# Kernel optimization log

Hardware: AMD Instinct MI355X
Metric: run time of the kernel (lower is better)

## Reference

```python
import jax, jax.numpy as jnp
import numpy as np

B, N, F_ = 4, 2048, 512
H = 8
D = F_ // H


def setup_inputs() -> dict:
    key = jax.random.key(0)
    ks = jax.random.split(key, 9)
    s = 1.0 / np.sqrt(F_)
    return {
        "x": jax.random.normal(ks[0], (B, N, F_), dtype=jnp.float32),
        "Wq": jax.random.normal(ks[1], (F_, F_), dtype=jnp.float32) * s,
        "bq": jax.random.normal(ks[2], (F_,), dtype=jnp.float32) * 0.01,
        "Wk": jax.random.normal(ks[3], (F_, F_), dtype=jnp.float32) * s,
        "bk": jax.random.normal(ks[4], (F_,), dtype=jnp.float32) * 0.01,
        "Wv": jax.random.normal(ks[5], (F_, F_), dtype=jnp.float32) * s,
        "bv": jax.random.normal(ks[6], (F_,), dtype=jnp.float32) * 0.01,
        "Wo": jax.random.normal(ks[7], (F_, F_), dtype=jnp.float32) * s,
        "bo": jax.random.normal(ks[8], (F_,), dtype=jnp.float32) * 0.01,
    }


def reference(x, Wq, bq, Wk, bk, Wv, bv, Wo, bo):
    b, n, f = x.shape
    h, d = H, f // H
    # projections -> [b, h, n, d]
    q = (x @ Wq + bq).reshape(b, n, h, d).transpose(0, 2, 1, 3)
    k = (x @ Wk + bk).reshape(b, n, h, d).transpose(0, 2, 1, 3)
    v = (x @ Wv + bv).reshape(b, n, h, d).transpose(0, 2, 1, 3)
    # NOTE: module scales by sqrt(feats), not sqrt(head_dim)
    sqrt_d = jnp.asarray(f, x.dtype) ** 0.5
    score = jax.nn.softmax(jnp.einsum('bhif,bhjf->bhij', q, k) / sqrt_d, axis=-1)
    attn = jnp.einsum('bhij,bhjf->bihf', score, v).reshape(b, n, f)
    return attn @ Wo + bo
```

## Files before the change

kernel.cpp:

```cpp
#include <hip/hip_runtime.h>


typedef _Float16 f16;
typedef _Float16 f16x2 __attribute__((ext_vector_type(2)));
typedef _Float16 f16x4 __attribute__((ext_vector_type(4)));
typedef _Float16 f16x8 __attribute__((ext_vector_type(8)));
typedef float f32x4 __attribute__((ext_vector_type(4)));

#define MFMA16(a, b, c) __builtin_amdgcn_mfma_f32_16x16x32_f16((a), (b), (c), 0, 0, 0)
#if __has_builtin(__builtin_amdgcn_exp2f)
#define EXP2(x) __builtin_amdgcn_exp2f(x)
#else
#define EXP2(x) exp2f(x)
#endif
#define GLLDS16(gp, lp)                                                    \
  __builtin_amdgcn_global_load_lds(                                        \
      (const __attribute__((address_space(1))) unsigned int*)(gp),         \
      (__attribute__((address_space(3))) unsigned int*)(lp), 16, 0, 0)

#define QSCALE 0.0637587f

__global__ __launch_bounds__(256) void k_cvt_x(const float* __restrict__ x,
                                               f16* __restrict__ xb, int n4) {
  int i = blockIdx.x * 256 + threadIdx.x;
  const int stride = gridDim.x * 256;
  const float4* xp = (const float4*)x;
  f16x4* op = (f16x4*)xb;
  for (; i < n4; i += stride) {
    float4 v = xp[i];
    f16x4 o = {(f16)v.x, (f16)v.y, (f16)v.z, (f16)v.w};
    op[i] = o;
  }
}

__global__ __launch_bounds__(256) void k_cvt_w(const float* __restrict__ Wq,
                                               const float* __restrict__ Wk,
                                               const float* __restrict__ Wv,
                                               const float* __restrict__ Wo,
                                               f16* __restrict__ wt) {
  const int w = blockIdx.y;
  const float* W = (w == 0) ? Wq : (w == 1) ? Wk : (w == 2) ? Wv : Wo;
  const int j0 = (blockIdx.x >> 4) * 32;
  const int k0 = (blockIdx.x & 15) * 32;
  __shared__ float tl[32][33];
  const int tx = threadIdx.x & 31, ty = threadIdx.x >> 5;
#pragma unroll
  for (int i = 0; i < 32; i += 8)
    tl[ty + i][tx] = W[(size_t)(k0 + ty + i) * 512 + j0 + tx];
  __syncthreads();
#pragma unroll
  for (int i = 0; i < 32; i += 8)
    wt[(size_t)w * 262144 + (size_t)(j0 + ty + i) * 512 + (k0 + tx)] =
        (f16)tl[tx][ty + i];
}

template <int BN, int MODE>
__global__ __launch_bounds__(256) void k_gemm(
    const f16* __restrict__ A, const f16* __restrict__ Wb3,
    const float* __restrict__ bias0, const float* __restrict__ bias1,
    const float* __restrict__ bias2, f16* __restrict__ oQ, f16* __restrict__ oK,
    f16* __restrict__ oV, float* __restrict__ oOut) {
  __shared__ __align__(16) f16 a_lds[128 * 64];
  __shared__ __align__(16) f16 b_lds[BN * 64];
  const int t = threadIdx.x;
  const int lane = t & 63, wid = t >> 6;
  const int l15 = lane & 15, l4 = lane >> 4;
  constexpr int MT = (BN == 128) ? 4 : 2;
  const int mbase = (BN == 128) ? (wid >> 1) * 64 : wid * 32;
  const int nbase = (BN == 128) ? (wid & 1) * 64 : 0;
  const int m0 = blockIdx.x * 128;
  const int by = blockIdx.y;
  const int wsel = (MODE == 0) ? (by >> 2) : 0;
  const int n0l = (MODE == 0) ? ((by & 3) * 128) : (by * (BN == 64 ? 64 : 128));
  const f16* Wt = Wb3 + (size_t)wsel * 262144;

  const int srow = t >> 3;
  const int sswz = ((t & 7) ^ (srow & 7)) * 8;
  const f16* Ag = A + (size_t)(m0 + srow) * 512 + sswz;
  const f16* Bg = Wt + (size_t)(n0l + srow) * 512 + sswz;

  f32x4 acc[MT][4];
  const f32x4 z4 = {0.f, 0.f, 0.f, 0.f};
#pragma unroll
  for (int i = 0; i < MT; i++)
#pragma unroll
    for (int j = 0; j < 4; j++) acc[i][j] = z4;

  for (int k0 = 0; k0 < 512; k0 += 64) {
#pragma unroll
    for (int i = 0; i < 4; i++)
      GLLDS16(Ag + (size_t)i * 16384 + k0, &a_lds[i * 2048 + wid * 512]);
#pragma unroll
    for (int i = 0; i < BN / 32; i++)
      GLLDS16(Bg + (size_t)i * 16384 + k0, &b_lds[i * 2048 + wid * 512]);
    __syncthreads();
#pragma unroll
    for (int ks = 0; ks < 2; ks++) {
      const int rs = ((ks * 4 + l4) ^ (l15 & 7)) * 8;
      f16x8 af[MT], bf[4];
#pragma unroll
      for (int mt = 0; mt < MT; mt++)
        af[mt] = *(const f16x8*)&a_lds[(mbase + mt * 16 + l15) * 64 + rs];
#pragma unroll
      for (int nt = 0; nt < 4; nt++)
        bf[nt] = *(const f16x8*)&b_lds[(nbase + nt * 16 + l15) * 64 + rs];
      __builtin_amdgcn_s_setprio(1);
#pragma unroll
      for (int mt = 0; mt < MT; mt++)
#pragma unroll
        for (int nt = 0; nt < 4; nt++)
          acc[mt][nt] = MFMA16(af[mt], bf[nt], acc[mt][nt]);
      __builtin_amdgcn_s_setprio(0);
    }
    __syncthreads();
  }

  if (MODE == 1) {
#pragma unroll
    for (int mt = 0; mt < MT; mt++)
#pragma unroll
      for (int nt = 0; nt < 4; nt++) {
        const int row = m0 + mbase + mt * 16 + l4 * 4;
        const int col = n0l + nbase + nt * 16 + l15;
        const float bv = bias0[col];
#pragma unroll
        for (int r = 0; r < 4; r++)
          oOut[(size_t)(row + r) * 512 + col] = acc[mt][nt][r] + bv;
      }
  } else {
#pragma unroll
    for (int mt = 0; mt < MT; mt++)
#pragma unroll
      for (int nt = 0; nt < 4; nt++) {
        const int colg = by * 128 + nbase + nt * 16 + l15;
        const int w = colg >> 9, jj = colg & 511;
        const int h = jj >> 6, d = jj & 63;
        const float* bp = (w == 0) ? bias0 : (w == 1) ? bias1 : bias2;
        const float bv = bp[jj];
        const float scl = (w == 0) ? QSCALE : 1.0f;
        const int rowg = m0 + mbase + mt * 16 + l4 * 4;
        const int b = rowg >> 11, nn = rowg & 2047;
        if (w == 2) {
          const size_t vb = ((size_t)(b * 8 + h) * 64 + d) * 2048 + nn;
#pragma unroll
          for (int r = 0; r < 4; r++)
            oV[vb + r] = (f16)(acc[mt][nt][r] + bv);
        } else {
          f16* op = (w == 0) ? oQ : oK;
          const size_t base = ((size_t)(b * 8 + h) * 2048 + nn) * 64 + d;
#pragma unroll
          for (int r = 0; r < 4; r++)
            op[base + (size_t)r * 64] = (f16)((acc[mt][nt][r] + bv) * scl);
        }
      }
  }
}

__global__ __launch_bounds__(128, 4) void k_attn(const f16* __restrict__ Q,
                                                 const f16* __restrict__ K,
                                                 const f16* __restrict__ Vt,
                                                 f16* __restrict__ CTX) {
  __shared__ __align__(16) f16 k_lds[2][4096];
  __shared__ __align__(16) f16 v_lds[2][4096];
  const int t = threadIdx.x, wid = t >> 6, lane = t & 63;
  const int l15 = lane & 15, l4 = lane >> 4;
  const int bid = blockIdx.x;
  const int bh = (bid & 7) * 4 + (bid >> 8);
  const int qb = (bid >> 3) & 31;
  const int q0 = qb * 64 + wid * 32;
  const size_t kvb = (size_t)bh * (2048 * 64);

  f16x8 qf[2][2];
#pragma unroll
  for (int g = 0; g < 2; g++)
#pragma unroll
    for (int ks = 0; ks < 2; ks++)
      qf[g][ks] = *(const f16x8*)&Q[kvb + (size_t)(q0 + g * 16 + l15) * 64 +
                                    ks * 32 + l4 * 8];

  f32x4 oa[2][4];
  f32x4 lacc[2];
  const f32x4 z4 = {0.f, 0.f, 0.f, 0.f};
#pragma unroll
  for (int g = 0; g < 2; g++) {
    lacc[g] = z4;
#pragma unroll
    for (int dt = 0; dt < 4; dt++) oa[g][dt] = z4;
  }
  const f16 one = (f16)1.0f;
  const f16x8 ones = {one, one, one, one, one, one, one, one};

  const int kswz = ((lane & 7) ^ (lane >> 3)) * 8;
  const f16* Kgp[4];
  const f16* Vgp[4];
#pragma unroll
  for (int i = 0; i < 4; i++) {
    const int L = i * 16 + wid * 8 + (lane >> 3);
    const int pr = (L & 0x20) | ((L & 0x0C) << 1) | ((L & 0x10) >> 2) | (L & 3);
    Kgp[i] = K + kvb + (size_t)pr * 64 + kswz;
    Vgp[i] = Vt + kvb + (size_t)L * 2048 + kswz;
  }

#pragma unroll
  for (int i = 0; i < 4; i++) {
    GLLDS16(Kgp[i], &k_lds[0][i * 1024 + wid * 512]);
    GLLDS16(Vgp[i], &v_lds[0][i * 1024 + wid * 512]);
  }
  __syncthreads();

  int cur = 0;
  for (int it = 0; it < 32; ++it) {
    if (it < 31) {
      const size_t kb = (size_t)(it + 1) * 4096;
      const size_t vb = (size_t)(it + 1) * 64;
#pragma unroll
      for (int i = 0; i < 4; i++) {
        GLLDS16(Kgp[i] + kb, &k_lds[cur ^ 1][i * 1024 + wid * 512]);
        GLLDS16(Vgp[i] + vb, &v_lds[cur ^ 1][i * 1024 + wid * 512]);
      }
    }

    f32x4 st[2][4];
#pragma unroll
    for (int g = 0; g < 2; g++)
#pragma unroll
      for (int w = 0; w < 4; w++) st[g][w] = z4;
    const f16* kl = k_lds[cur];
#pragma unroll
    for (int ks = 0; ks < 2; ks++) {
      const int rs = ((ks * 4 + l4) ^ (l15 & 7)) * 8;
      f16x8 kf[4];
#pragma unroll
      for (int w = 0; w < 4; w++)
        kf[w] = *(const f16x8*)&kl[(w * 16 + l15) * 64 + rs];
      __builtin_amdgcn_s_setprio(1);
#pragma unroll
      for (int w = 0; w < 4; w++) {
        st[0][w] = MFMA16(kf[w], qf[0][ks], st[0][w]);
        st[1][w] = MFMA16(kf[w], qf[1][ks], st[1][w]);
      }
      __builtin_amdgcn_s_setprio(0);
    }

    f16x8 pa[2][2];
#pragma unroll
    for (int g = 0; g < 2; g++)
#pragma unroll
      for (int ks = 0; ks < 2; ks++) {
        f16x2 a0 = __builtin_bit_cast(
            f16x2, __builtin_amdgcn_cvt_pkrtz(EXP2(st[g][2 * ks][0]),
                                              EXP2(st[g][2 * ks][1])));
        f16x2 a1 = __builtin_bit_cast(
            f16x2, __builtin_amdgcn_cvt_pkrtz(EXP2(st[g][2 * ks][2]),
                                              EXP2(st[g][2 * ks][3])));
        f16x2 a2 = __builtin_bit_cast(
            f16x2, __builtin_amdgcn_cvt_pkrtz(EXP2(st[g][2 * ks + 1][0]),
                                              EXP2(st[g][2 * ks + 1][1])));
        f16x2 a3 = __builtin_bit_cast(
            f16x2, __builtin_amdgcn_cvt_pkrtz(EXP2(st[g][2 * ks + 1][2]),
                                              EXP2(st[g][2 * ks + 1][3])));
        f16x8 p;
        p[0] = a0[0]; p[1] = a0[1]; p[2] = a1[0]; p[3] = a1[1];
        p[4] = a2[0]; p[5] = a2[1]; p[6] = a3[0]; p[7] = a3[1];
        pa[g][ks] = p;
      }

    const f16* vl = v_lds[cur];
#pragma unroll
    for (int ks = 0; ks < 2; ks++) {
      __builtin_amdgcn_s_setprio(1);
      lacc[0] = MFMA16(pa[0][ks], ones, lacc[0]);
      lacc[1] = MFMA16(pa[1][ks], ones, lacc[1]);
#pragma unroll
      for (int dt = 0; dt < 4; dt++) {
        const f16x8 vf = *(const f16x8*)&vl[(dt * 16 + l15) * 64 +
                                            ((ks * 4 + l4) ^ (l15 & 7)) * 8];
        oa[0][dt] = MFMA16(pa[0][ks], vf, oa[0][dt]);
        oa[1][dt] = MFMA16(pa[1][ks], vf, oa[1][dt]);
      }
      __builtin_amdgcn_s_setprio(0);
    }
    __syncthreads();
    cur ^= 1;
  }

  const int b = bh >> 3, h = bh & 7;
#pragma unroll
  for (int g = 0; g < 2; g++)
#pragma unroll
    for (int r = 0; r < 4; r++) {
      const float inv = 1.0f / lacc[g][r];
      const int qrow = q0 + g * 16 + l4 * 4 + r;
#pragma unroll
      for (int dt = 0; dt < 4; dt++)
        CTX[(size_t)(b * 2048 + qrow) * 512 + h * 64 + dt * 16 + l15] =
            (f16)(oa[g][dt][r] * inv);
    }
}

extern "C" void kernel_launch(void* const* d_in, const int* in_sizes, int n_in,
                              void* d_out, int out_size, void* d_ws,
                              size_t ws_size, hipStream_t stream) {
  const float* x = (const float*)d_in[0];
  const float* Wq = (const float*)d_in[1];
  const float* bq = (const float*)d_in[2];
  const float* Wk = (const float*)d_in[3];
  const float* bk = (const float*)d_in[4];
  const float* Wv = (const float*)d_in[5];
  const float* bv = (const float*)d_in[6];
  const float* Wo = (const float*)d_in[7];
  const float* bo = (const float*)d_in[8];
  float* out = (float*)d_out;
  char* ws = (char*)d_ws;

  f16* xb = (f16*)(ws);
  f16* wt = (f16*)(ws + (size_t)(8u << 20));
  f16* Qb = (f16*)(ws + (size_t)(10u << 20));
  f16* Kb = (f16*)(ws + (size_t)(18u << 20));
  f16* Vt = (f16*)(ws + (size_t)(26u << 20));
  f16* CX = (f16*)(ws + (size_t)(34u << 20));

  k_cvt_x<<<dim3(2048), dim3(256), 0, stream>>>(x, xb, 1048576);
  k_cvt_w<<<dim3(256, 4), dim3(256), 0, stream>>>(Wq, Wk, Wv, Wo, wt);
  k_gemm<128, 0><<<dim3(64, 12), dim3(256), 0, stream>>>(
      xb, wt, bq, bk, bv, Qb, Kb, Vt, nullptr);
  k_attn<<<dim3(1024), dim3(128), 0, stream>>>(Qb, Kb, Vt, CX);
  k_gemm<64, 1><<<dim3(64, 8), dim3(256), 0, stream>>>(
      CX, wt + (size_t)3 * 262144, bo, nullptr, nullptr, nullptr, nullptr,
      nullptr, out);
}
```

Before: 96.95 us.

## Split attention KV range across two wave groups and reduce partials via LDS

```diff
diff --git a/kernel.cpp b/kernel.cpp
--- a/kernel.cpp
+++ b/kernel.cpp
@@ -156,19 +156,21 @@
   }
 }
 
-__global__ __launch_bounds__(128, 4) void k_attn(const f16* __restrict__ Q,
+__global__ __launch_bounds__(512, 4) void k_attn(const f16* __restrict__ Q,
                                                  const f16* __restrict__ K,
                                                  const f16* __restrict__ Vt,
                                                  f16* __restrict__ CTX) {
-  __shared__ __align__(16) f16 k_lds[2][4096];
-  __shared__ __align__(16) f16 v_lds[2][4096];
+  __shared__ __align__(16) f16 k_lds[2][2][4096];
+  __shared__ __align__(16) f16 v_lds[2][2][4096];
   const int t = threadIdx.x, wid = t >> 6, lane = t & 63;
   const int l15 = lane & 15, l4 = lane >> 4;
+  const int s = wid >> 2, w4 = wid & 3;
   const int bid = blockIdx.x;
-  const int bh = (bid & 7) * 4 + (bid >> 8);
-  const int qb = (bid >> 3) & 31;
-  const int q0 = qb * 64 + wid * 32;
+  const int bh = (bid & 7) * 4 + (bid >> 7);
+  const int qb = (bid >> 3) & 15;
+  const int q0 = qb * 128 + w4 * 32;
   const size_t kvb = (size_t)bh * (2048 * 64);
+  const int kv0 = s * 1024;
 
   f16x8 qf[2][2];
 #pragma unroll
@@ -190,34 +192,27 @@
   const f16 one = (f16)1.0f;
   const f16x8 ones = {one, one, one, one, one, one, one, one};
 
+  const int krow = w4 * 8 + (lane >> 3);
   const int kswz = ((lane & 7) ^ (lane >> 3)) * 8;
-  const f16* Kgp[4];
-  const f16* Vgp[4];
-#pragma unroll
-  for (int i = 0; i < 4; i++) {
-    const int L = i * 16 + wid * 8 + (lane >> 3);
-    const int pr = (L & 0x20) | ((L & 0x0C) << 1) | ((L & 0x10) >> 2) | (L & 3);
-    Kgp[i] = K + kvb + (size_t)pr * 64 + kswz;
-    Vgp[i] = Vt + kvb + (size_t)L * 2048 + kswz;
-  }
-
-#pragma unroll
-  for (int i = 0; i < 4; i++) {
-    GLLDS16(Kgp[i], &k_lds[0][i * 1024 + wid * 512]);
-    GLLDS16(Vgp[i], &v_lds[0][i * 1024 + wid * 512]);
-  }
+  const int kperm = ((krow & 0x0C) << 1) | ((krow & 0x10) >> 2) | (krow & 3);
+  const f16* Kg = K + kvb + (size_t)(kv0 + kperm) * 64 + kswz;
+  const f16* Vg = Vt + kvb + (size_t)krow * 2048 + kv0 + kswz;
+
+  GLLDS16(Kg, &k_lds[s][0][w4 * 512]);
+  GLLDS16(Kg + 2048, &k_lds[s][0][w4 * 512 + 2048]);
+  GLLDS16(Vg, &v_lds[s][0][w4 * 512]);
+  GLLDS16(Vg + 32 * 2048, &v_lds[s][0][w4 * 512 + 2048]);
   __syncthreads();
 
   int cur = 0;
-  for (int it = 0; it < 32; ++it) {
-    if (it < 31) {
+  for (int it = 0; it < 16; ++it) {
+    if (it < 15) {
       const size_t kb = (size_t)(it + 1) * 4096;
       const size_t vb = (size_t)(it + 1) * 64;
-#pragma unroll
-      for (int i = 0; i < 4; i++) {
-        GLLDS16(Kgp[i] + kb, &k_lds[cur ^ 1][i * 1024 + wid * 512]);
-        GLLDS16(Vgp[i] + vb, &v_lds[cur ^ 1][i * 1024 + wid * 512]);
-      }
+      GLLDS16(Kg + kb, &k_lds[s][cur ^ 1][w4 * 512]);
+      GLLDS16(Kg + kb + 2048, &k_lds[s][cur ^ 1][w4 * 512 + 2048]);
+      GLLDS16(Vg + vb, &v_lds[s][cur ^ 1][w4 * 512]);
+      GLLDS16(Vg + vb + 32 * 2048, &v_lds[s][cur ^ 1][w4 * 512 + 2048]);
     }
 
     f32x4 st[2][4];
@@ -225,7 +220,7 @@
     for (int g = 0; g < 2; g++)
 #pragma unroll
       for (int w = 0; w < 4; w++) st[g][w] = z4;
-    const f16* kl = k_lds[cur];
+    const f16* kl = &k_lds[s][cur][0];
 #pragma unroll
     for (int ks = 0; ks < 2; ks++) {
       const int rs = ((ks * 4 + l4) ^ (l15 & 7)) * 8;
@@ -265,7 +260,7 @@
         pa[g][ks] = p;
       }
 
-    const f16* vl = v_lds[cur];
+    const f16* vl = &v_lds[s][cur][0];
 #pragma unroll
     for (int ks = 0; ks < 2; ks++) {
       __builtin_amdgcn_s_setprio(1);
@@ -284,18 +279,41 @@
     cur ^= 1;
   }
 
-  const int b = bh >> 3, h = bh & 7;
-#pragma unroll
-  for (int g = 0; g < 2; g++)
-#pragma unroll
-    for (int r = 0; r < 4; r++) {
-      const float inv = 1.0f / lacc[g][r];
-      const int qrow = q0 + g * 16 + l4 * 4 + r;
+  float* so = (float*)&k_lds[0][0][0];
+  float* sl = (float*)&v_lds[0][0][0];
+  const int ln = w4 * 64 + lane;
+  if (s == 1) {
+#pragma unroll
+    for (int g = 0; g < 2; g++) {
 #pragma unroll
       for (int dt = 0; dt < 4; dt++)
-        CTX[(size_t)(b * 2048 + qrow) * 512 + h * 64 + dt * 16 + l15] =
-            (f16)(oa[g][dt][r] * inv);
-    }
+#pragma unroll
+        for (int r = 0; r < 4; r++)
+          so[(g * 16 + dt * 4 + r) * 256 + ln] = oa[g][dt][r];
+#pragma unroll
+      for (int r = 0; r < 4; r++) sl[(g * 4 + r) * 256 + ln] = lacc[g][r];
+    }
+  }
+  __syncthreads();
+  if (s == 0) {
+    const int b = bh >> 3, h = bh & 7;
+#pragma unroll
+    for (int g = 0; g < 2; g++) {
+#pragma unroll
+      for (int r = 0; r < 4; r++) {
+        const float lt = lacc[g][r] + sl[(g * 4 + r) * 256 + ln];
+        const float inv = 1.0f / lt;
+        const int qrow = q0 + g * 16 + l4 * 4 + r;
+#pragma unroll
+        for (int dt = 0; dt < 4; dt++) {
+          const float ov =
+              oa[g][dt][r] + so[(g * 16 + dt * 4 + r) * 256 + ln];
+          CTX[(size_t)(b * 2048 + qrow) * 512 + h * 64 + dt * 16 + l15] =
+              (f16)(ov * inv);
+        }
+      }
+    }
+  }
 }
 
 extern "C" void kernel_launch(void* const* d_in, const int* in_sizes, int n_in,
@@ -324,7 +342,7 @@
   k_cvt_w<<<dim3(256, 4), dim3(256), 0, stream>>>(Wq, Wk, Wv, Wo, wt);
   k_gemm<128, 0><<<dim3(64, 12), dim3(256), 0, stream>>>(
       xb, wt, bq, bk, bv, Qb, Kb, Vt, nullptr);
-  k_attn<<<dim3(1024), dim3(128), 0, stream>>>(Qb, Kb, Vt, CX);
+  k_attn<<<dim3(512), dim3(512), 0, stream>>>(Qb, Kb, Vt, CX);
   k_gemm<64, 1><<<dim3(64, 8), dim3(256), 0, stream>>>(
       CX, wt + (size_t)3 * 262144, bo, nullptr, nullptr, nullptr, nullptr,
       nullptr, out);
```

Result: faster. 81.99 us (-15.4%).
